# Optimization experiments

Measured on AMD Instinct MI355X. Metric: run time of the kernel, lower is better.

## Reference

```python
import jax, jax.numpy as jnp
import numpy as np

CAMS, HEADS, PTS, LAYERS = 6, 8, 2, 3
D, DH, FFN = 256, 32, 512
VZ, VH, VW = 8, 50, 50
NQ = VZ * VH * VW
IN_C = 768
IMG_H, IMG_W = 256, 704
FH, FW = IMG_H // 32, IMG_W // 32   # 8, 22
L = FH * FW                         # 176 tokens per camera
LVIS = 44                           # visible tokens (mask_ratio=0.75)


def _layer_norm(x, g, b, eps=1e-5):
    m = x.mean(-1, keepdims=True)
    v = x.var(-1, keepdims=True)
    return (x - m) / jnp.sqrt(v + eps) * g + b


def _group_norm(x, g, b, groups=16, eps=1e-5):
    B, C = x.shape[0], x.shape[1]
    xg = x.reshape(B, groups, C // groups, *x.shape[2:])
    m = xg.mean(axis=(2, 3, 4, 5), keepdims=True)
    v = xg.var(axis=(2, 3, 4, 5), keepdims=True)
    xg = (xg - m) / jnp.sqrt(v + eps)
    return xg.reshape(x.shape) * g[None, :, None, None, None] + b[None, :, None, None, None]


def _bilinear(val, loc, Hf, Wf):
    # val: [C, HW, heads, dh]; loc: [C, NQ, heads, P, 2] as (x, y) pixel coords
    x, y = loc[..., 0], loc[..., 1]
    x0 = jnp.floor(x); y0 = jnp.floor(y)
    wx, wy = x - x0, y - y0
    x0i, y0i = x0.astype(jnp.int32), y0.astype(jnp.int32)
    cidx = jnp.arange(val.shape[0])[:, None, None, None]
    hidx = jnp.arange(val.shape[2])[None, None, :, None]

    def g(yi, xi):
        idx = jnp.clip(yi, 0, Hf - 1) * Wf + jnp.clip(xi, 0, Wf - 1)
        return val[cidx, idx, hidx]  # [C,NQ,heads,P,dh]

    out = ((1 - wx) * (1 - wy))[..., None] * g(y0i, x0i)
    out = out + (wx * (1 - wy))[..., None] * g(y0i, x0i + 1)
    out = out + ((1 - wx) * wy)[..., None] * g(y0i + 1, x0i)
    out = out + (wx * wy)[..., None] * g(y0i + 1, x0i + 1)
    return out


def setup_inputs() -> dict:
    key = jax.random.key(0)
    ks = iter(jax.random.split(key, 48))

    def rn(shape, s=0.02):
        return jax.random.normal(next(ks), shape, jnp.float32) * s

    return {
        'camera_x': jax.random.normal(next(ks), (CAMS, LVIS, IN_C), jnp.float32),
        'camera_ids_restore': jax.random.randint(next(ks), (CAMS, L), 0, L),
        'img_h': IMG_H, 'img_w': IMG_W,
        'mask_token': rn((1, 1, IN_C)),
        'vol_emb': rn((NQ, D), 1.0),
        'W_tc': rn((D, IN_C)), 'b_tc': jnp.zeros((D,), jnp.float32),
        'cams_embeds': rn((CAMS, D), 1.0),
        'level_embeds': rn((1, D), 1.0),
        'W_off': rn((LAYERS, D, HEADS * CAMS * PTS * 2)),
        'b_off': rn((LAYERS, HEADS * CAMS * PTS * 2), 2.0),
        'W_att': rn((LAYERS, D, HEADS * CAMS * PTS)),
        'b_att': jnp.zeros((LAYERS, HEADS * CAMS * PTS), jnp.float32),
        'W_val': rn((LAYERS, D, D)), 'b_val': jnp.zeros((LAYERS, D), jnp.float32),
        'W_out': rn((LAYERS, D, D)), 'b_out': jnp.zeros((LAYERS, D), jnp.float32),
        'ln1_g': jnp.ones((LAYERS, D), jnp.float32), 'ln1_b': jnp.zeros((LAYERS, D), jnp.float32),
        'W_ff1': rn((LAYERS, D, FFN)), 'b_ff1': jnp.zeros((LAYERS, FFN), jnp.float32),
        'W_ff2': rn((LAYERS, FFN, D)), 'b_ff2': jnp.zeros((LAYERS, D), jnp.float32),
        'ln2_g': jnp.ones((LAYERS, D), jnp.float32), 'ln2_b': jnp.zeros((LAYERS, D), jnp.float32),
        'deconv_w': rn((D, D, 2, 2, 2)),
        'gn1_g': jnp.ones((D,), jnp.float32), 'gn1_b': jnp.zeros((D,), jnp.float32),
        'conv3_w': rn((192, D, 3, 3, 3)),
        'gn2_g': jnp.ones((192,), jnp.float32), 'gn2_b': jnp.zeros((192,), jnp.float32),
    }


def _forward(camera_x, camera_ids_restore, img_h, img_w, mask_token, vol_emb, W_tc, b_tc,
             cams_embeds, level_embeds, W_off, b_off, W_att, b_att, W_val, b_val, W_out, b_out,
             ln1_g, ln1_b, W_ff1, b_ff1, W_ff2, b_ff2, ln2_g, ln2_b,
             deconv_w, gn1_g, gn1_b, conv3_w, gn2_g, gn2_b):
    N, Lfull = camera_ids_restore.shape
    # 1) MAE unshuffle: append mask tokens, gather back to original order
    mt = jnp.broadcast_to(mask_token, (N, Lfull - camera_x.shape[1], IN_C)).astype(camera_x.dtype)
    full = jnp.concatenate([camera_x, mt], axis=1)                         # [N,L,C]
    full = jnp.take_along_axis(full, camera_ids_restore[:, :, None], axis=1)
    Hf, Wf = img_h // 32, img_w // 32
    cam_x = jnp.transpose(full, (0, 2, 1)).reshape(1, N, IN_C, Hf, Wf)     # [1,6,768,8,22]
    # 2) 1x1 transfer conv + ReLU
    vf = jax.nn.relu(jnp.einsum('bnchw,oc->bnohw', cam_x, W_tc) + b_tc[None, None, :, None, None])
    # 3) flatten spatial + cam/level embeds -> per-camera feature maps [N,HW,D]
    vf = jnp.transpose(vf.reshape(1, N, D, Hf * Wf), (1, 0, 3, 2))          # [N,1,HW,D]
    vf = vf + cams_embeds[:, None, None, :] + level_embeds[None, None, 0:1, :]
    feat = vf[:, 0]                                                         # [N,HW,D]
    # 4) reference points of volume queries (z slow, h, w fast) -> pixel coords
    ww = (jnp.arange(VW, dtype=jnp.float32) + 0.5) / VW
    hh = (jnp.arange(VH, dtype=jnp.float32) + 0.5) / VH
    grid = jnp.stack([jnp.tile(ww, VH), jnp.repeat(hh, VW)], axis=-1)       # [VH*VW,2]
    ref_pix = jnp.tile(grid, (VZ, 1)) * jnp.array([Wf, Hf], jnp.float32) - 0.5  # [NQ,2]
    # 5) deformable cross-attention volume encoder
    q = vol_emb
    for l in range(LAYERS):
        off = (q @ W_off[l] + b_off[l]).reshape(NQ, HEADS, CAMS, PTS, 2)
        att = jax.nn.softmax((q @ W_att[l] + b_att[l]).reshape(NQ, HEADS, CAMS * PTS), axis=-1)
        att = jnp.transpose(att.reshape(NQ, HEADS, CAMS, PTS), (2, 0, 1, 3))      # [C,NQ,H,P]
        val = (feat @ W_val[l] + b_val[l]).reshape(CAMS, Hf * Wf, HEADS, DH)
        loc = jnp.transpose(ref_pix[:, None, None, None, :] + off, (2, 0, 1, 3, 4))  # [C,NQ,H,P,2]
        sampled = _bilinear(val, loc, Hf, Wf)                                     # [C,NQ,H,P,DH]
        agg = jnp.einsum('cnhp,cnhpd->nhd', att, sampled).reshape(NQ, D)
        q = _layer_norm(q + agg @ W_out[l] + b_out[l], ln1_g[l], ln1_b[l])
        q = _layer_norm(q + jax.nn.relu(q @ W_ff1[l] + b_ff1[l]) @ W_ff2[l] + b_ff2[l], ln2_g[l], ln2_b[l])
    # 6) reshape -> [1, D, VW, VH, VZ] (matches .permute(0,4,3,2,1))
    vol = jnp.transpose(q.reshape(1, VZ, VH, VW, D), (0, 4, 3, 2, 1))
    # 7) deblock: deconv3d(k=2,s=2) -> GN16 -> ReLU -> conv3d(k=3,p=1) -> GN16 -> ReLU
    x = jax.lax.conv_transpose(vol, deconv_w, (2, 2, 2), 'VALID',
                               dimension_numbers=('NCDHW', 'OIDHW', 'NCDHW'))
    x = jax.nn.relu(_group_norm(x, gn1_g, gn1_b))
    x = jax.lax.conv_general_dilated(x, conv3_w, (1, 1, 1), [(1, 1)] * 3,
                                     dimension_numbers=('NCDHW', 'OIDHW', 'NCDHW'))
    x = jax.nn.relu(_group_norm(x, gn2_g, gn2_b))
    return x, cam_x


def reference(camera_x, camera_ids_restore, img_h, img_w, mask_token, vol_emb, W_tc, b_tc,
              cams_embeds, level_embeds, W_off, b_off, W_att, b_att, W_val, b_val, W_out, b_out,
              ln1_g, ln1_b, W_ff1, b_ff1, W_ff2, b_ff2, ln2_g, ln2_b,
              deconv_w, gn1_g, gn1_b, conv3_w, gn2_g, gn2_b):
    return _forward(camera_x, camera_ids_restore, img_h, img_w, mask_token, vol_emb, W_tc, b_tc,
                    cams_embeds, level_embeds, W_off, b_off, W_att, b_att, W_val, b_val, W_out, b_out,
                    ln1_g, ln1_b, W_ff1, b_ff1, W_ff2, b_ff2, ln2_g, ln2_b,
                    deconv_w, gn1_g, gn1_b, conv3_w, gn2_g, gn2_b)
```

## Files before the change

### kernel.cpp

```cpp
#include <hip/hip_runtime.h>
#include <stdint.h>

typedef __attribute__((ext_vector_type(8))) short s16x8;
typedef __attribute__((ext_vector_type(4))) float f32x4;

static __device__ __forceinline__ unsigned short f2bf(float f) {
  unsigned u = __float_as_uint(f);
  u += 0x7FFFu + ((u >> 16) & 1u);
  return (unsigned short)(u >> 16);
}
static __device__ __forceinline__ float bf2f(unsigned short h) {
  return __uint_as_float(((unsigned)h) << 16);
}
static __device__ __forceinline__ void sum8(uint4 u, float& a, float& q) {
  unsigned w[4] = {u.x, u.y, u.z, u.w};
#pragma unroll
  for (int i = 0; i < 4; ++i) {
    float v0 = __uint_as_float((w[i] & 0xFFFFu) << 16);
    float v1 = __uint_as_float(w[i] & 0xFFFF0000u);
    a += v0 + v1;
    q += v0 * v0 + v1 * v1;
  }
}

__global__ void k_prep(const float* __restrict__ W_tc, const float* __restrict__ W_val,
                       const float* __restrict__ W_off, const float* __restrict__ W_att,
                       const float* __restrict__ W_out, const float* __restrict__ W_ff1,
                       const float* __restrict__ W_ff2, const float* __restrict__ deconv_w,
                       const float* __restrict__ conv3_w,
                       unsigned short* __restrict__ Wt_tc, unsigned short* __restrict__ Wt_val,
                       unsigned short* __restrict__ Wt_oa, unsigned short* __restrict__ Wt_out,
                       unsigned short* __restrict__ Wt_ff1, unsigned short* __restrict__ Wt_ff2,
                       unsigned short* __restrict__ Wt_dc, unsigned short* __restrict__ wc3) {
  int idx = blockIdx.x * 256 + threadIdx.x;
  if (idx < 196608) { Wt_tc[idx] = f2bf(W_tc[idx]); return; }
  idx -= 196608;
  if (idx < 196608) {
    int l = idx / 65536, r = idx - l * 65536, k = r >> 8, n = r & 255;
    Wt_val[l * 65536 + n * 256 + k] = f2bf(W_val[l * 65536 + r]);
    return;
  }
  idx -= 196608;
  if (idx < 147456) {
    int l = idx / 49152, r = idx - l * 49152, k = r / 192, n = r - k * 192;
    Wt_oa[l * 73728 + n * 256 + k] = f2bf(W_off[l * 49152 + r]);
    return;
  }
  idx -= 147456;
  if (idx < 73728) {
    int l = idx / 24576, r = idx - l * 24576, k = r / 96, n = r - k * 96;
    Wt_oa[l * 73728 + 192 * 256 + n * 256 + k] = f2bf(W_att[l * 24576 + r]);
    return;
  }
  idx -= 73728;
  if (idx < 196608) {
    int l = idx / 65536, r = idx - l * 65536, k = r >> 8, n = r & 255;
    Wt_out[l * 65536 + n * 256 + k] = f2bf(W_out[l * 65536 + r]);
    return;
  }
  idx -= 196608;
  if (idx < 393216) {
    int l = idx / 131072, r = idx - l * 131072, k = r >> 9, n = r & 511;
    Wt_ff1[l * 131072 + n * 256 + k] = f2bf(W_ff1[l * 131072 + r]);
    return;
  }
  idx -= 393216;
  if (idx < 393216) {
    int l = idx / 131072, r = idx - l * 131072, k = r >> 8, n = r & 255;
    Wt_ff2[l * 131072 + n * 512 + k] = f2bf(W_ff2[l * 131072 + r]);
    return;
  }
  idx -= 393216;
  if (idx < 524288) {
    int n = idx >> 8, k = idx & 255;
    Wt_dc[idx] = f2bf(deconv_w[(size_t)(n & 255) * 2048 + k * 8 + (n >> 8)]);
    return;
  }
  idx -= 524288;
  if (idx < 1327104) {
    int tap = idx / 49152;
    int rem = idx - tap * 49152;
    int oc = rem >> 8, ic = rem & 255;
    int chunk = ic >> 5, kg = (ic >> 3) & 3, j = ic & 7;
    int ocblk = oc >> 4, lo = oc & 15;
    size_t frag = (size_t)(tap * 8 + chunk) * 12 + ocblk;
    wc3[(frag * 64 + kg * 16 + lo) * 8 + j] = f2bf(conv3_w[(oc * 256 + ic) * 27 + tap]);
    return;
  }
}

__global__ void k_cvt(const float* __restrict__ in, unsigned short* __restrict__ out, int n) {
  int i = blockIdx.x * 256 + threadIdx.x;
  if (i < n) out[i] = f2bf(in[i]);
}

__global__ void k_restore2(const float* __restrict__ cx, const int* __restrict__ ids,
                           const float* __restrict__ mtok, float* __restrict__ out_camx,
                           unsigned short* __restrict__ camxT) {
  int idx = blockIdx.x * 256 + threadIdx.x;
  if (idx >= 811008) return;
  int ch = idx % 768;
  int row = idx / 768;
  int c = row / 176, p = row - c * 176;
  int id = ids[c * 176 + p];
  float v = (id < 44) ? cx[((size_t)(c * 44 + id)) * 768 + ch] : mtok[ch];
  camxT[idx] = f2bf(v);
  out_camx[((size_t)(c * 768 + ch)) * 176 + p] = v;
}

template <int MODE>
__global__ __launch_bounds__(256) void k_gemm(
    const unsigned short* __restrict__ A, int M, int lda,
    const unsigned short* __restrict__ Bt, int K, int N,
    const float* __restrict__ bias, const float* __restrict__ bias2, int n1, int relu,
    float* __restrict__ Cf, unsigned short* __restrict__ Cb, int ldc,
    const float* __restrict__ cemb, const float* __restrict__ lemb) {
  __shared__ short sA[128 * 40];
  const int t = threadIdx.x;
  const int l = t & 63, w = t >> 6;
  const int lo = l & 15, kg = l >> 4;
  const int row0 = blockIdx.x * 128, n0 = blockIdx.y * 64;
  const s16x8 bz = {0, 0, 0, 0, 0, 0, 0, 0};
  f32x4 acc[2][4] = {};
  s16x8 bc[4], bn[4];
#pragma unroll
  for (int nb = 0; nb < 4; ++nb) {
    int n = n0 + nb * 16 + lo;
    bc[nb] = (n < N) ? *(const s16x8*)&Bt[(size_t)n * K + kg * 8] : bz;
  }
  const int stR = t >> 1, stH = t & 1;
  for (int kc = 0; kc < K; kc += 32) {
    const bool pf = (kc + 32 < K);
    if (pf) {
#pragma unroll
      for (int nb = 0; nb < 4; ++nb) {
        int n = n0 + nb * 16 + lo;
        bn[nb] = (n < N) ? *(const s16x8*)&Bt[(size_t)n * K + kc + 32 + kg * 8] : bz;
      }
    }
    __syncthreads();
    {
      int r = row0 + stR;
      uint4 v0 = {0u, 0u, 0u, 0u}, v1 = {0u, 0u, 0u, 0u};
      if (r < M) {
        const unsigned short* src = A + (size_t)r * lda + kc + stH * 16;
        v0 = *(const uint4*)src;
        v1 = *(const uint4*)(src + 8);
      }
      *(uint4*)&sA[stR * 40 + stH * 16] = v0;
      *(uint4*)&sA[stR * 40 + stH * 16 + 8] = v1;
    }
    __syncthreads();
    s16x8 a0 = *(const s16x8*)&sA[(w * 32 + lo) * 40 + kg * 8];
    s16x8 a1 = *(const s16x8*)&sA[(w * 32 + 16 + lo) * 40 + kg * 8];
#pragma unroll
    for (int nb = 0; nb < 4; ++nb) {
      acc[0][nb] = __builtin_amdgcn_mfma_f32_16x16x32_bf16(a0, bc[nb], acc[0][nb], 0, 0, 0);
      acc[1][nb] = __builtin_amdgcn_mfma_f32_16x16x32_bf16(a1, bc[nb], acc[1][nb], 0, 0, 0);
    }
    if (pf) {
#pragma unroll
      for (int nb = 0; nb < 4; ++nb) bc[nb] = bn[nb];
    }
  }
#pragma unroll
  for (int m = 0; m < 2; ++m)
#pragma unroll
    for (int nb = 0; nb < 4; ++nb)
#pragma unroll
      for (int r = 0; r < 4; ++r) {
        int row = row0 + w * 32 + m * 16 + (kg << 2) + r;
        int col = n0 + nb * 16 + lo;
        if (row < M && col < N) {
          float v = acc[m][nb][r];
          if (bias) v += (col < n1) ? bias[col] : bias2[col - n1];
          if (relu) v = fmaxf(v, 0.f);
          if (MODE == 0) {
            Cf[(size_t)row * ldc + col] = v;
          } else if (MODE == 2) {
            Cb[(size_t)row * ldc + col] = f2bf(v);
          } else {
            v += cemb[(row / 176) * 256 + col] + lemb[col];
            Cb[(size_t)row * ldc + col] = f2bf(v);
          }
        }
      }
}

__global__ __launch_bounds__(256, 2) void k_deconv(const unsigned short* __restrict__ A,
                                                   const unsigned short* __restrict__ Bt,
                                                   unsigned short* __restrict__ Cb, int M) {
  __shared__ short sA[128 * 256];
  const int t = threadIdx.x;
  const int l = t & 63, w = t >> 6;
  const int lo = l & 15, kg = l >> 4;
  const int row0 = blockIdx.x * 128;
#pragma unroll
  for (int i = 0; i < 16; ++i) {
    int g = t + i * 256;
    int row = g >> 5, gcol = g & 31;
    int r = row0 + row;
    uint4 v = {0u, 0u, 0u, 0u};
    if (r < M) v = *(const uint4*)&A[(size_t)r * 256 + gcol * 8];
    *(uint4*)&sA[row * 256 + ((gcol ^ (row & 7)) << 3)] = v;
  }
  __syncthreads();
  const int r0 = w * 32 + lo, r1 = r0 + 16;
  for (int nt = 0; nt < 32; ++nt) {
    f32x4 acc[2][4] = {};
    s16x8 bc[4], bn[4];
    const int ncol0 = nt * 64;
#pragma unroll
    for (int nb = 0; nb < 4; ++nb)
      bc[nb] = *(const s16x8*)&Bt[(size_t)(ncol0 + nb * 16 + lo) * 256 + kg * 8];
#pragma unroll
    for (int kc = 0; kc < 8; ++kc) {
      const bool pf = kc < 7;
      if (pf) {
#pragma unroll
        for (int nb = 0; nb < 4; ++nb)
          bn[nb] = *(const s16x8*)&Bt[(size_t)(ncol0 + nb * 16 + lo) * 256 + (kc + 1) * 32 + kg * 8];
      }
      int g0 = kc * 4 + kg;
      s16x8 a0 = *(const s16x8*)&sA[r0 * 256 + ((g0 ^ (r0 & 7)) << 3)];
      s16x8 a1 = *(const s16x8*)&sA[r1 * 256 + ((g0 ^ (r1 & 7)) << 3)];
#pragma unroll
      for (int nb = 0; nb < 4; ++nb) {
        acc[0][nb] = __builtin_amdgcn_mfma_f32_16x16x32_bf16(a0, bc[nb], acc[0][nb], 0, 0, 0);
        acc[1][nb] = __builtin_amdgcn_mfma_f32_16x16x32_bf16(a1, bc[nb], acc[1][nb], 0, 0, 0);
      }
      if (pf) {
#pragma unroll
        for (int nb = 0; nb < 4; ++nb) bc[nb] = bn[nb];
      }
    }
    const int tap = nt >> 2;
    const int t1 = tap >> 2, t2 = (tap >> 1) & 1, t3 = tap & 1;
#pragma unroll
    for (int m = 0; m < 2; ++m)
#pragma unroll
      for (int nb = 0; nb < 4; ++nb)
#pragma unroll
        for (int r = 0; r < 4; ++r) {
          int row = row0 + w * 32 + m * 16 + (kg << 2) + r;
          if (row < M) {
            int oc = (nt & 3) * 64 + nb * 16 + lo;
            int z = row / 2500, rr = row - z * 2500;
            int hy = rr / 50, wx = rr - hy * 50;
            int od = 2 * wx + 1 - t1, oh = 2 * hy + 1 - t2, ow = 2 * z + 1 - t3;
            Cb[((size_t)((od * 100 + oh) * 16 + ow)) * 256 + oc] = f2bf(acc[m][nb][r]);
          }
        }
  }
}

__global__ __launch_bounds__(256) void k_sample(const float* __restrict__ oa,
                                                const float* __restrict__ val,
                                                unsigned short* __restrict__ aggb) {
  __shared__ float sl[96], sw[96];
  int t = threadIdx.x;
  int h = t >> 5, d = t & 31;
  const float* vbh0 = val + (size_t)h * 32 + d;
  for (int r = 0; r < 8; ++r) {
    int n = blockIdx.x * 8 + r;
    if (t < 96) sl[t] = oa[(size_t)n * 288 + 192 + t];
    __syncthreads();
    if (t < 96) {
      int hh = t / 12;
      float mx = -1e30f;
#pragma unroll
      for (int j = 0; j < 12; ++j) mx = fmaxf(mx, sl[hh * 12 + j]);
      sw[t] = __expf(sl[t] - mx);
    }
    __syncthreads();
    float ssum = 0.f;
#pragma unroll
    for (int j = 0; j < 12; ++j) ssum += sw[h * 12 + j];
    float inv = 1.f / ssum;
    float xr = ((float)(n % 50) + 0.5f) * (22.0f / 50.0f) - 0.5f;
    float yr = ((float)((n / 50) % 50) + 0.5f) * (8.0f / 50.0f) - 0.5f;
    float acc = 0.f;
    const float* offn = oa + (size_t)n * 288 + h * 24;
#pragma unroll
    for (int c = 0; c < 6; ++c)
#pragma unroll
      for (int p2 = 0; p2 < 2; ++p2) {
        float x = xr + offn[(c * 2 + p2) * 2];
        float y = yr + offn[(c * 2 + p2) * 2 + 1];
        float x0 = floorf(x), y0 = floorf(y);
        float wx = x - x0, wy = y - y0;
        int ix0 = min(max((int)x0, 0), 21), ix1 = min(max((int)x0 + 1, 0), 21);
        int iy0 = min(max((int)y0, 0), 7), iy1 = min(max((int)y0 + 1, 0), 7);
        const float* vb = vbh0 + (size_t)c * 176 * 768;
        float v00 = vb[(size_t)(iy0 * 22 + ix0) * 768];
        float v01 = vb[(size_t)(iy0 * 22 + ix1) * 768];
        float v10 = vb[(size_t)(iy1 * 22 + ix0) * 768];
        float v11 = vb[(size_t)(iy1 * 22 + ix1) * 768];
        float bil = (1.f - wx) * (1.f - wy) * v00 + wx * (1.f - wy) * v01 +
                    (1.f - wx) * wy * v10 + wx * wy * v11;
        acc += sw[h * 12 + c * 2 + p2] * inv * bil;
      }
    aggb[(size_t)n * 256 + t] = f2bf(acc);
    __syncthreads();
  }
}

__global__ __launch_bounds__(256) void k_addln(float* __restrict__ q, const float* __restrict__ p,
                                               const float* __restrict__ g, const float* __restrict__ b,
                                               unsigned short* __restrict__ qb) {
  __shared__ float red[8];
  int t = threadIdx.x;
  int w = t >> 6;
  float gg = g[t], bb = b[t];
  for (int r = 0; r < 8; ++r) {
    size_t n = (size_t)blockIdx.x * 8 + r;
    float x = q[n * 256 + t] + p[n * 256 + t];
    float s1 = x, s2 = x * x;
#pragma unroll
    for (int o = 32; o >= 1; o >>= 1) {
      s1 += __shfl_xor(s1, o, 64);
      s2 += __shfl_xor(s2, o, 64);
    }
    if ((t & 63) == 0) { red[w * 2] = s1; red[w * 2 + 1] = s2; }
    __syncthreads();
    s1 = red[0] + red[2] + red[4] + red[6];
    s2 = red[1] + red[3] + red[5] + red[7];
    float mean = s1 * (1.0f / 256.0f);
    float var = s2 * (1.0f / 256.0f) - mean * mean;
    float y = (x - mean) * rsqrtf(var + 1e-5f) * gg + bb;
    q[n * 256 + t] = y;
    qb[n * 256 + t] = f2bf(y);
    __syncthreads();
  }
}

__global__ __launch_bounds__(256) void k_gnstat1(const unsigned short* __restrict__ X, float* __restrict__ part) {
  __shared__ float s1[256], s2[256];
  int b = blockIdx.x, t = threadIdx.x;
  int oc8 = t & 31, v0 = t >> 5;
  float a = 0.f, q = 0.f;
#pragma unroll
  for (int i = 0; i < 8; ++i) {
    int vox = v0 + i * 8;
    uint4 u = *(const uint4*)&X[(size_t)b * 16384 + vox * 256 + oc8 * 8];
    sum8(u, a, q);
  }
  s1[t] = a; s2[t] = q;
  __syncthreads();
  if (t < 128) { s1[t] += s1[t + 128]; s2[t] += s2[t + 128]; }
  __syncthreads();
  if (t < 64) { s1[t] += s1[t + 64]; s2[t] += s2[t + 64]; }
  __syncthreads();
  if (t < 32) { s1[t] += s1[t + 32]; s2[t] += s2[t + 32]; }
  __syncthreads();
  if (t < 16) {
    part[t * 2500 + b] = s1[2 * t] + s1[2 * t + 1];
    part[40000 + t * 2500 + b] = s2[2 * t] + s2[2 * t + 1];
  }
}

__global__ __launch_bounds__(256) void k_gnred1(const float* __restrict__ part, float* __restrict__ gmv) {
  __shared__ float s1[256], s2[256];
  int g = blockIdx.x, t = threadIdx.x;
  float a = 0.f, q = 0.f;
  for (int i = t; i < 2500; i += 256) { a += part[g * 2500 + i]; q += part[40000 + g * 2500 + i]; }
  s1[t] = a; s2[t] = q;
  __syncthreads();
  for (int s = 128; s > 0; s >>= 1) {
    if (t < s) { s1[t] += s1[t + s]; s2[t] += s2[t + s]; }
    __syncthreads();
  }
  if (t == 0) {
    float m = s1[0] / 2560000.0f;
    float v = s2[0] / 2560000.0f - m * m;
    gmv[2 * g] = m; gmv[2 * g + 1] = rsqrtf(v + 1e-5f);
  }
}

__global__ __launch_bounds__(256) void k_gnapply1(unsigned short* __restrict__ X, const float* __restrict__ gmv,
                                                  const float* __restrict__ g, const float* __restrict__ b) {
  for (unsigned i = blockIdx.x * 256 + threadIdx.x; i < 5120000u; i += gridDim.x * 256) {
    unsigned e = i * 8u;
    int oc0 = e & 255, grp = oc0 >> 4;
    float mean = gmv[grp * 2], rstd = gmv[grp * 2 + 1];
    float4 g0 = *(const float4*)&g[oc0], g1 = *(const float4*)&g[oc0 + 4];
    float4 b0 = *(const float4*)&b[oc0], b1 = *(const float4*)&b[oc0 + 4];
    uint4 u = *(const uint4*)&X[e];
    unsigned w[4] = {u.x, u.y, u.z, u.w};
    float gg[8] = {g0.x, g0.y, g0.z, g0.w, g1.x, g1.y, g1.z, g1.w};
    float bb[8] = {b0.x, b0.y, b0.z, b0.w, b1.x, b1.y, b1.z, b1.w};
    unsigned o[4];
#pragma unroll
    for (int j = 0; j < 4; ++j) {
      float v0 = __uint_as_float((w[j] & 0xFFFFu) << 16);
      float v1 = __uint_as_float(w[j] & 0xFFFF0000u);
      v0 = fmaxf((v0 - mean) * rstd * gg[2 * j] + bb[2 * j], 0.f);
      v1 = fmaxf((v1 - mean) * rstd * gg[2 * j + 1] + bb[2 * j + 1], 0.f);
      o[j] = (unsigned)f2bf(v0) | ((unsigned)f2bf(v1) << 16);
    }
    *(uint4*)&X[e] = make_uint4(o[0], o[1], o[2], o[3]);
  }
}

__global__ __launch_bounds__(256, 2) void k_conv3(const unsigned short* __restrict__ X,
                                                  const unsigned short* __restrict__ Wp,
                                                  unsigned short* __restrict__ Y) {
  __shared__ short sX[4 * 543 * 8];
  int bid = blockIdx.x;
  int xcd = bid & 7, idx = bid >> 3;
  int swz = (xcd < 4 ? xcd * 163 : 652 + (xcd - 4) * 162) + idx;
  const int od = swz / 13;
  const int oh0 = (swz - od * 13) * 8;
  const int t = threadIdx.x;
  const int l = t & 63, w = t >> 6;
  const int kg = l >> 4, lo = l & 15;
  f32x4 acc[8][3] = {};
  s16x8 bc[9], bn[9];
  const unsigned short* Wl = Wp + (size_t)l * 8;
  const int w3 = w * 3;
#pragma unroll
  for (int t2 = 0; t2 < 3; ++t2)
#pragma unroll
    for (int nb = 0; nb < 3; ++nb)
      bc[t2 * 3 + nb] = *(const s16x8*)&Wl[(size_t)((t2 * 3 * 8) * 12 + w3 + nb) * 512];

  for (int gi = 0; gi < 72; ++gi) {
    const int chunk = gi / 9;
    const int sub = gi - chunk * 9;
    const int t1 = sub / 3, t3 = sub - t1 * 3;
    if (sub == 0) {
      __syncthreads();
#pragma unroll
      for (int i = 0; i < 9; ++i) {
        int e = t + i * 256;
        if (e < 2160) {
          int pos = e >> 2, ks = e & 3;
          int sd = pos / 180, r2 = pos - sd * 180;
          int sh = r2 / 18, sw_ = r2 - sh * 18;
          int gd = od + sd - 1, gh = oh0 + sh - 1, gw = sw_ - 1;
          uint4 v = {0u, 0u, 0u, 0u};
          if ((unsigned)gd < 100u && (unsigned)gh < 100u && (unsigned)gw < 16u)
            v = *(const uint4*)&X[((size_t)((gd * 100 + gh) * 16 + gw)) * 256 + chunk * 32 + ks * 8];
          *(uint4*)&sX[(ks * 543 + pos) * 8] = v;
        }
      }
      __syncthreads();
    }
    const int gn1 = gi + 1;
    if (gn1 < 72) {
      const int c1 = gn1 / 9, su1 = gn1 - c1 * 9;
      const int t1n = su1 / 3, t3n = su1 - t1n * 3;
#pragma unroll
      for (int t2 = 0; t2 < 3; ++t2)
#pragma unroll
        for (int nb = 0; nb < 3; ++nb)
          bn[t2 * 3 + nb] = *(const s16x8*)&Wl[
              (size_t)(((t1n * 9 + t2 * 3 + t3n) * 8 + c1) * 12 + w3 + nb) * 512];
    }
    const int abase = kg * 543 + t1 * 180 + lo + t3;
#pragma unroll
    for (int sh = 0; sh < 10; ++sh) {
      s16x8 a = *(const s16x8*)&sX[(abase + sh * 18) * 8];
#pragma unroll
      for (int t2 = 0; t2 < 3; ++t2) {
        const int m = sh - t2;
        if (m >= 0 && m < 8) {
          acc[m][0] = __builtin_amdgcn_mfma_f32_16x16x32_bf16(a, bc[t2 * 3 + 0], acc[m][0], 0, 0, 0);
          acc[m][1] = __builtin_amdgcn_mfma_f32_16x16x32_bf16(a, bc[t2 * 3 + 1], acc[m][1], 0, 0, 0);
          acc[m][2] = __builtin_amdgcn_mfma_f32_16x16x32_bf16(a, bc[t2 * 3 + 2], acc[m][2], 0, 0, 0);
        }
      }
    }
#pragma unroll
    for (int i = 0; i < 9; ++i) bc[i] = bn[i];
  }
#pragma unroll
  for (int m = 0; m < 8; ++m) {
    int oh = oh0 + m;
    if (oh < 100) {
#pragma unroll
      for (int nb = 0; nb < 3; ++nb)
#pragma unroll
        for (int r = 0; r < 4; ++r) {
          int oc = w * 48 + nb * 16 + lo;
          int ow = (kg << 2) + r;
          Y[(size_t)oc * 160000 + (size_t)((od * 100 + oh) * 16) + ow] = f2bf(acc[m][nb][r]);
        }
    }
  }
}

__global__ __launch_bounds__(256) void k_gnstat2(const unsigned short* __restrict__ X, float* __restrict__ part) {
  __shared__ float s1[256], s2[256];
  int b = blockIdx.x, t = threadIdx.x;
  int ch = b / 10, pp = b - ch * 10;
  const unsigned short* base = X + (size_t)ch * 160000 + (size_t)pp * 16000;
  float a = 0.f, q = 0.f;
  for (int i = t; i < 2000; i += 256) {
    uint4 u = *(const uint4*)&base[i * 8];
    sum8(u, a, q);
  }
  s1[t] = a; s2[t] = q;
  __syncthreads();
  for (int s = 128; s > 0; s >>= 1) {
    if (t < s) { s1[t] += s1[t + s]; s2[t] += s2[t + s]; }
    __syncthreads();
  }
  if (t == 0) { part[80000 + ch * 10 + pp] = s1[0]; part[81920 + ch * 10 + pp] = s2[0]; }
}

__global__ __launch_bounds__(256) void k_gnred2(const float* __restrict__ part, float* __restrict__ gmv) {
  __shared__ float s1[256], s2[256];
  int g = blockIdx.x, t = threadIdx.x;
  float a = (t < 120) ? part[80000 + g * 120 + t] : 0.f;
  float q = (t < 120) ? part[81920 + g * 120 + t] : 0.f;
  s1[t] = a; s2[t] = q;
  __syncthreads();
  for (int s = 128; s > 0; s >>= 1) {
    if (t < s) { s1[t] += s1[t + s]; s2[t] += s2[t + s]; }
    __syncthreads();
  }
  if (t == 0) {
    float m = s1[0] / 1920000.0f;
    float v = s2[0] / 1920000.0f - m * m;
    gmv[2 * g] = m; gmv[2 * g + 1] = rsqrtf(v + 1e-5f);
  }
}

__global__ __launch_bounds__(256) void k_gnapply2(const unsigned short* __restrict__ X, const float* __restrict__ gmv,
                                                  const float* __restrict__ g, const float* __restrict__ b,
                                                  float* __restrict__ out) {
  for (unsigned i = blockIdx.x * 256 + threadIdx.x; i < 3840000u; i += gridDim.x * 256) {
    unsigned oc = i / 20000u;
    unsigned grp = oc / 12u;
    float mean = gmv[grp * 2], rstd = gmv[grp * 2 + 1];
    float gam = g[oc], bet = b[oc];
    unsigned e = i * 8u;
    uint4 u = *(const uint4*)&X[e];
    unsigned wv[4] = {u.x, u.y, u.z, u.w};
    float o[8];
#pragma unroll
    for (int j = 0; j < 4; ++j) {
      float v0 = __uint_as_float((wv[j] & 0xFFFFu) << 16);
      float v1 = __uint_as_float(wv[j] & 0xFFFF0000u);
      o[2 * j] = fmaxf((v0 - mean) * rstd * gam + bet, 0.f);
      o[2 * j + 1] = fmaxf((v1 - mean) * rstd * gam + bet, 0.f);
    }
    *(float4*)&out[e] = make_float4(o[0], o[1], o[2], o[3]);
    *(float4*)&out[e + 4] = make_float4(o[4], o[5], o[6], o[7]);
  }
}

static inline dim3 gemm_grid(int M, int N) { return dim3((M + 127) / 128, (N + 63) / 64); }

extern "C" void kernel_launch(void* const* d_in, const int* in_sizes, int n_in,
                              void* d_out, int out_size, void* d_ws, size_t ws_size,
                              hipStream_t stream) {
  const float* camera_x = (const float*)d_in[0];
  const int* ids = (const int*)d_in[1];
  const float* mask_tok = (const float*)d_in[4];
  const float* vol_emb = (const float*)d_in[5];
  const float* W_tc = (const float*)d_in[6];
  const float* b_tc = (const float*)d_in[7];
  const float* cams_emb = (const float*)d_in[8];
  const float* lvl_emb = (const float*)d_in[9];
  const float* W_off = (const float*)d_in[10];
  const float* b_off = (const float*)d_in[11];
  const float* W_att = (const float*)d_in[12];
  const float* b_att = (const float*)d_in[13];
  const float* W_val = (const float*)d_in[14];
  const float* b_val = (const float*)d_in[15];
  const float* W_out = (const float*)d_in[16];
  const float* b_out = (const float*)d_in[17];
  const float* ln1_g = (const float*)d_in[18];
  const float* ln1_b = (const float*)d_in[19];
  const float* W_ff1 = (const float*)d_in[20];
  const float* b_ff1 = (const float*)d_in[21];
  const float* W_ff2 = (const float*)d_in[22];
  const float* b_ff2 = (const float*)d_in[23];
  const float* ln2_g = (const float*)d_in[24];
  const float* ln2_b = (const float*)d_in[25];
  const float* deconv_w = (const float*)d_in[26];
  const float* gn1_g = (const float*)d_in[27];
  const float* gn1_b = (const float*)d_in[28];
  const float* conv3_w = (const float*)d_in[29];
  const float* gn2_g = (const float*)d_in[30];
  const float* gn2_b = (const float*)d_in[31];

  char* ws = (char*)d_ws;
  float* q             = (float*)(ws + 0);
  unsigned short* qb   = (unsigned short*)(ws + 20480000);
  float* proj          = (float*)(ws + 30720000);
  float* oa            = (float*)(ws + 51200000);
  unsigned short* aggb = (unsigned short*)(ws + 74240000);
  unsigned short* ffhb = (unsigned short*)(ws + 84480000);
  float* val3          = (float*)(ws + 104960000);
  unsigned short* featb= (unsigned short*)(ws + 108204032);
  unsigned short* x1bf = (unsigned short*)(ws + 30720000);
  unsigned short* c3   = (unsigned short*)(ws + 112640000);
  unsigned short* Wt_val = (unsigned short*)(ws + 174080000);
  unsigned short* Wt_oa  = (unsigned short*)(ws + 174473216);
  unsigned short* Wt_out = (unsigned short*)(ws + 174915584);
  unsigned short* Wt_ff1 = (unsigned short*)(ws + 175308800);
  unsigned short* Wt_ff2 = (unsigned short*)(ws + 176095232);
  unsigned short* Wt_dc  = (unsigned short*)(ws + 176881664);
  unsigned short* wc3    = (unsigned short*)(ws + 177930240);
  float* part = (float*)(ws + 180584448);
  float* gmv1 = (float*)(ws + 180920320);
  float* gmv2 = (float*)(ws + 180920448);
  unsigned short* Wt_tc  = (unsigned short*)(ws + 180920576);
  unsigned short* camxT  = (unsigned short*)(ws + 181707008);

  float* out_x = (float*)d_out;
  float* out_camx = out_x + 30720000;

  k_prep<<<13472, 256, 0, stream>>>(W_tc, W_val, W_off, W_att, W_out, W_ff1, W_ff2,
                                    deconv_w, conv3_w,
                                    Wt_tc, Wt_val, Wt_oa, Wt_out, Wt_ff1, Wt_ff2, Wt_dc, wc3);

  k_restore2<<<3168, 256, 0, stream>>>(camera_x, ids, mask_tok, out_camx, camxT);
  k_gemm<4><<<gemm_grid(1056, 256), 256, 0, stream>>>(camxT, 1056, 768, Wt_tc, 768, 256,
                                                      b_tc, nullptr, 256, 1, nullptr, featb, 256,
                                                      cams_emb, lvl_emb);
  hipMemcpyAsync(q, vol_emb, (size_t)20000 * 256 * 4, hipMemcpyDeviceToDevice, stream);
  k_cvt<<<20000, 256, 0, stream>>>(vol_emb, qb, 5120000);

  k_gemm<0><<<gemm_grid(1056, 768), 256, 0, stream>>>(featb, 1056, 256, Wt_val, 256, 768,
                                                      b_val, nullptr, 768, 0, val3, nullptr, 768,
                                                      nullptr, nullptr);

  for (int lyr = 0; lyr < 3; ++lyr) {
    k_gemm<0><<<gemm_grid(20000, 288), 256, 0, stream>>>(qb, 20000, 256, Wt_oa + lyr * 73728, 256, 288,
                                                         b_off + lyr * 192, b_att + lyr * 96, 192, 0,
                                                         oa, nullptr, 288, nullptr, nullptr);
    k_sample<<<2500, 256, 0, stream>>>(oa, val3 + lyr * 256, aggb);
    k_gemm<0><<<gemm_grid(20000, 256), 256, 0, stream>>>(aggb, 20000, 256, Wt_out + lyr * 65536, 256, 256,
                                                         b_out + lyr * 256, nullptr, 256, 0,
                                                         proj, nullptr, 256, nullptr, nullptr);
    k_addln<<<2500, 256, 0, stream>>>(q, proj, ln1_g + lyr * 256, ln1_b + lyr * 256, qb);
    k_gemm<2><<<gemm_grid(20000, 512), 256, 0, stream>>>(qb, 20000, 256, Wt_ff1 + lyr * 131072, 256, 512,
                                                         b_ff1 + lyr * 512, nullptr, 512, 1,
                                                         nullptr, ffhb, 512, nullptr, nullptr);
    k_gemm<0><<<gemm_grid(20000, 256), 256, 0, stream>>>(ffhb, 20000, 512, Wt_ff2 + lyr * 131072, 512, 256,
                                                         b_ff2 + lyr * 256, nullptr, 256, 0,
                                                         proj, nullptr, 256, nullptr, nullptr);
    k_addln<<<2500, 256, 0, stream>>>(q, proj, ln2_g + lyr * 256, ln2_b + lyr * 256, qb);
  }

  k_deconv<<<157, 256, 0, stream>>>(qb, Wt_dc, x1bf, 20000);

  k_gnstat1<<<2500, 256, 0, stream>>>(x1bf, part);
  k_gnred1<<<16, 256, 0, stream>>>(part, gmv1);
  k_gnapply1<<<2048, 256, 0, stream>>>(x1bf, gmv1, gn1_g, gn1_b);

  k_conv3<<<1300, 256, 0, stream>>>(x1bf, wc3, c3);

  k_gnstat2<<<1920, 256, 0, stream>>>(c3, part);
  k_gnred2<<<16, 256, 0, stream>>>(part, gmv2);
  k_gnapply2<<<2048, 256, 0, stream>>>(c3, gmv2, gn2_g, gn2_b, out_x);
}
```

Baseline: 1.431 ms.

## Fuse output/FFN2 GEMMs with residual add and LayerNorm

Adds a GEMM kernel that computes a full 256-wide output row tile per block, then applies bias, residual add and LayerNorm in registers before writing q and its bf16 copy. This replaces the separate GEMM-to-proj plus add-LN kernels for both projections in every layer, removing the fp32 proj round trip and a launch. The first layer reads vol_emb directly as the residual, which also drops the initial device copy. The risks are lower occupancy from 64 accumulators per thread, B operands streamed from global memory with no shared staging, and only 313 blocks in the grid.

Result: slower. 1.600 ms (+11.8%).

```diff
diff --git a/kernel.cpp b/kernel.cpp
--- a/kernel.cpp
+++ b/kernel.cpp
@@ -187,6 +187,104 @@
       }
 }
 
+template <int KT>
+__global__ __launch_bounds__(256) void k_gemmln(
+    const unsigned short* __restrict__ A, int M,
+    const unsigned short* __restrict__ Bt,
+    const float* __restrict__ bias,
+    const float* __restrict__ qin,
+    const float* __restrict__ g, const float* __restrict__ b,
+    float* __restrict__ qout, unsigned short* __restrict__ qbout) {
+  __shared__ short sA[64 * (KT + 8)];
+  const int t = threadIdx.x;
+  const int l = t & 63, w = t >> 6;
+  const int lo = l & 15, kg = l >> 4;
+  const int row0 = blockIdx.x * 64;
+  f32x4 acc[16] = {};
+#pragma unroll
+  for (int i = 0; i < KT / 32; ++i) {
+    int gr = t + i * 256;
+    int row = gr / (KT / 8), c8 = gr - row * (KT / 8);
+    int r = row0 + row;
+    uint4 v = {0u, 0u, 0u, 0u};
+    if (r < M) v = *(const uint4*)&A[(size_t)r * KT + c8 * 8];
+    *(uint4*)&sA[row * (KT + 8) + c8 * 8] = v;
+  }
+  __syncthreads();
+  const int arow = (w * 16 + lo) * (KT + 8);
+#pragma unroll
+  for (int h = 0; h < 2; ++h) {
+    s16x8 bc[8], bn[8];
+#pragma unroll
+    for (int nb = 0; nb < 8; ++nb)
+      bc[nb] = *(const s16x8*)&Bt[(size_t)(h * 128 + nb * 16 + lo) * KT + kg * 8];
+#pragma unroll
+    for (int kc = 0; kc < KT; kc += 32) {
+      const bool pf = (kc + 32 < KT);
+      if (pf) {
+#pragma unroll
+        for (int nb = 0; nb < 8; ++nb)
+          bn[nb] = *(const s16x8*)&Bt[(size_t)(h * 128 + nb * 16 + lo) * KT + kc + 32 + kg * 8];
+      }
+      s16x8 a = *(const s16x8*)&sA[arow + kc + kg * 8];
+#pragma unroll
+      for (int nb = 0; nb < 8; ++nb)
+        acc[h * 8 + nb] = __builtin_amdgcn_mfma_f32_16x16x32_bf16(a, bc[nb], acc[h * 8 + nb], 0, 0, 0);
+      if (pf) {
+#pragma unroll
+        for (int nb = 0; nb < 8; ++nb) bc[nb] = bn[nb];
+      }
+    }
+  }
+  float s1[4] = {0.f, 0.f, 0.f, 0.f}, s2[4] = {0.f, 0.f, 0.f, 0.f};
+#pragma unroll
+  for (int h = 0; h < 2; ++h)
+#pragma unroll
+    for (int nb = 0; nb < 8; ++nb) {
+      int col = h * 128 + nb * 16 + lo;
+      float bs = bias[col];
+#pragma unroll
+      for (int r = 0; r < 4; ++r) {
+        int row = row0 + w * 16 + (kg << 2) + r;
+        float v = acc[h * 8 + nb][r] + bs;
+        if (row < M) v += qin[(size_t)row * 256 + col];
+        acc[h * 8 + nb][r] = v;
+        s1[r] += v;
+        s2[r] += v * v;
+      }
+    }
+#pragma unroll
+  for (int o = 8; o >= 1; o >>= 1)
+#pragma unroll
+    for (int r = 0; r < 4; ++r) {
+      s1[r] += __shfl_xor(s1[r], o, 64);
+      s2[r] += __shfl_xor(s2[r], o, 64);
+    }
+  float mean[4], rstd[4];
+#pragma unroll
+  for (int r = 0; r < 4; ++r) {
+    mean[r] = s1[r] * (1.0f / 256.0f);
+    float var = s2[r] * (1.0f / 256.0f) - mean[r] * mean[r];
+    rstd[r] = rsqrtf(var + 1e-5f);
+  }
+#pragma unroll
+  for (int h = 0; h < 2; ++h)
+#pragma unroll
+    for (int nb = 0; nb < 8; ++nb) {
+      int col = h * 128 + nb * 16 + lo;
+      float gg = g[col], bb = b[col];
+#pragma unroll
+      for (int r = 0; r < 4; ++r) {
+        int row = row0 + w * 16 + (kg << 2) + r;
+        if (row < M) {
+          float y = (acc[h * 8 + nb][r] - mean[r]) * rstd[r] * gg + bb;
+          qout[(size_t)row * 256 + col] = y;
+          qbout[(size_t)row * 256 + col] = f2bf(y);
+        }
+      }
+    }
+}
+
 __global__ __launch_bounds__(256, 2) void k_deconv(const unsigned short* __restrict__ A,
                                                    const unsigned short* __restrict__ Bt,
                                                    unsigned short* __restrict__ Cb, int M) {
@@ -301,35 +399,6 @@
         acc += sw[h * 12 + c * 2 + p2] * inv * bil;
       }
     aggb[(size_t)n * 256 + t] = f2bf(acc);
-    __syncthreads();
-  }
-}
-
-__global__ __launch_bounds__(256) void k_addln(float* __restrict__ q, const float* __restrict__ p,
-                                               const float* __restrict__ g, const float* __restrict__ b,
-                                               unsigned short* __restrict__ qb) {
-  __shared__ float red[8];
-  int t = threadIdx.x;
-  int w = t >> 6;
-  float gg = g[t], bb = b[t];
-  for (int r = 0; r < 8; ++r) {
-    size_t n = (size_t)blockIdx.x * 8 + r;
-    float x = q[n * 256 + t] + p[n * 256 + t];
-    float s1 = x, s2 = x * x;
-#pragma unroll
-    for (int o = 32; o >= 1; o >>= 1) {
-      s1 += __shfl_xor(s1, o, 64);
-      s2 += __shfl_xor(s2, o, 64);
-    }
-    if ((t & 63) == 0) { red[w * 2] = s1; red[w * 2 + 1] = s2; }
-    __syncthreads();
-    s1 = red[0] + red[2] + red[4] + red[6];
-    s2 = red[1] + red[3] + red[5] + red[7];
-    float mean = s1 * (1.0f / 256.0f);
-    float var = s2 * (1.0f / 256.0f) - mean * mean;
-    float y = (x - mean) * rsqrtf(var + 1e-5f) * gg + bb;
-    q[n * 256 + t] = y;
-    qb[n * 256 + t] = f2bf(y);
     __syncthreads();
   }
 }
@@ -590,7 +659,6 @@
   char* ws = (char*)d_ws;
   float* q             = (float*)(ws + 0);
   unsigned short* qb   = (unsigned short*)(ws + 20480000);
-  float* proj          = (float*)(ws + 30720000);
   float* oa            = (float*)(ws + 51200000);
   unsigned short* aggb = (unsigned short*)(ws + 74240000);
   unsigned short* ffhb = (unsigned short*)(ws + 84480000);
@@ -622,7 +690,6 @@
   k_gemm<4><<<gemm_grid(1056, 256), 256, 0, stream>>>(camxT, 1056, 768, Wt_tc, 768, 256,
                                                       b_tc, nullptr, 256, 1, nullptr, featb, 256,
                                                       cams_emb, lvl_emb);
-  hipMemcpyAsync(q, vol_emb, (size_t)20000 * 256 * 4, hipMemcpyDeviceToDevice, stream);
   k_cvt<<<20000, 256, 0, stream>>>(vol_emb, qb, 5120000);
 
   k_gemm<0><<<gemm_grid(1056, 768), 256, 0, stream>>>(featb, 1056, 256, Wt_val, 256, 768,
@@ -634,17 +701,14 @@
                                                          b_off + lyr * 192, b_att + lyr * 96, 192, 0,
                                                          oa, nullptr, 288, nullptr, nullptr);
     k_sample<<<2500, 256, 0, stream>>>(oa, val3 + lyr * 256, aggb);
-    k_gemm<0><<<gemm_grid(20000, 256), 256, 0, stream>>>(aggb, 20000, 256, Wt_out + lyr * 65536, 256, 256,
-                                                         b_out + lyr * 256, nullptr, 256, 0,
-                                                         proj, nullptr, 256, nullptr, nullptr);
-    k_addln<<<2500, 256, 0, stream>>>(q, proj, ln1_g + lyr * 256, ln1_b + lyr * 256, qb);
+    k_gemmln<256><<<313, 256, 0, stream>>>(aggb, 20000, Wt_out + lyr * 65536, b_out + lyr * 256,
+                                           (lyr == 0) ? vol_emb : q,
+                                           ln1_g + lyr * 256, ln1_b + lyr * 256, q, qb);
     k_gemm<2><<<gemm_grid(20000, 512), 256, 0, stream>>>(qb, 20000, 256, Wt_ff1 + lyr * 131072, 256, 512,
                                                          b_ff1 + lyr * 512, nullptr, 512, 1,
                                                          nullptr, ffhb, 512, nullptr, nullptr);
-    k_gemm<0><<<gemm_grid(20000, 256), 256, 0, stream>>>(ffhb, 20000, 512, Wt_ff2 + lyr * 131072, 512, 256,
-                                                         b_ff2 + lyr * 256, nullptr, 256, 0,
-                                                         proj, nullptr, 256, nullptr, nullptr);
-    k_addln<<<2500, 256, 0, stream>>>(q, proj, ln2_g + lyr * 256, ln2_b + lyr * 256, qb);
+    k_gemmln<512><<<313, 256, 0, stream>>>(ffhb, 20000, Wt_ff2 + lyr * 131072, b_ff2 + lyr * 256,
+                                           q, ln2_g + lyr * 256, ln2_b + lyr * 256, q, qb);
   }
 
   k_deconv<<<157, 256, 0, stream>>>(qb, Wt_dc, x1bf, 20000);
```

## Fuse GroupNorm statistics into deconv and conv3 epilogues via atomics

Applied to the files above, without the earlier changes.

Computes the per-group sum and sum of squares for both GroupNorms inside the deconv and conv3 epilogues. Partials are reduced within each wave and block, then atomically added to a small global accumulator. A tiny finalize kernel replaces the separate stat and reduce kernels. This drops two full re-reads of the large bf16 intermediates and four launches. In exchange it adds atomic contention, extra registers in the GEMM epilogues, and float atomics that make the summation order nondeterministic.

Result: slower. 1.501 ms (+4.9%).

```diff
diff --git a/kernel.cpp b/kernel.cpp
--- a/kernel.cpp
+++ b/kernel.cpp
@@ -11,16 +11,6 @@
 }
 static __device__ __forceinline__ float bf2f(unsigned short h) {
   return __uint_as_float(((unsigned)h) << 16);
-}
-static __device__ __forceinline__ void sum8(uint4 u, float& a, float& q) {
-  unsigned w[4] = {u.x, u.y, u.z, u.w};
-#pragma unroll
-  for (int i = 0; i < 4; ++i) {
-    float v0 = __uint_as_float((w[i] & 0xFFFFu) << 16);
-    float v1 = __uint_as_float(w[i] & 0xFFFF0000u);
-    a += v0 + v1;
-    q += v0 * v0 + v1 * v1;
-  }
 }
 
 __global__ void k_prep(const float* __restrict__ W_tc, const float* __restrict__ W_val,
@@ -92,6 +82,16 @@
 __global__ void k_cvt(const float* __restrict__ in, unsigned short* __restrict__ out, int n) {
   int i = blockIdx.x * 256 + threadIdx.x;
   if (i < n) out[i] = f2bf(in[i]);
+}
+
+__global__ void k_zero(float* __restrict__ p) { p[threadIdx.x] = 0.f; }
+
+__global__ void k_gnfin(const float* __restrict__ acc, float* __restrict__ gmv, float inv_n) {
+  int t = threadIdx.x;
+  float m = acc[2 * t] * inv_n;
+  float v = acc[2 * t + 1] * inv_n - m * m;
+  gmv[2 * t] = m;
+  gmv[2 * t + 1] = rsqrtf(v + 1e-5f);
 }
 
 __global__ void k_restore2(const float* __restrict__ cx, const int* __restrict__ ids,
@@ -189,7 +189,8 @@
 
 __global__ __launch_bounds__(256, 2) void k_deconv(const unsigned short* __restrict__ A,
                                                    const unsigned short* __restrict__ Bt,
-                                                   unsigned short* __restrict__ Cb, int M) {
+                                                   unsigned short* __restrict__ Cb, int M,
+                                                   float* __restrict__ gnacc) {
   __shared__ short sA[128 * 256];
   const int t = threadIdx.x;
   const int l = t & 63, w = t >> 6;
@@ -206,52 +207,75 @@
   }
   __syncthreads();
   const int r0 = w * 32 + lo, r1 = r0 + 16;
-  for (int nt = 0; nt < 32; ++nt) {
-    f32x4 acc[2][4] = {};
-    s16x8 bc[4], bn[4];
-    const int ncol0 = nt * 64;
-#pragma unroll
-    for (int nb = 0; nb < 4; ++nb)
-      bc[nb] = *(const s16x8*)&Bt[(size_t)(ncol0 + nb * 16 + lo) * 256 + kg * 8];
-#pragma unroll
-    for (int kc = 0; kc < 8; ++kc) {
-      const bool pf = kc < 7;
-      if (pf) {
+  float gs1[16], gs2[16];
+#pragma unroll
+  for (int g = 0; g < 16; ++g) { gs1[g] = 0.f; gs2[g] = 0.f; }
+  for (int ntH = 0; ntH < 8; ++ntH) {
+#pragma unroll
+    for (int ntL = 0; ntL < 4; ++ntL) {
+      const int nt = ntH * 4 + ntL;
+      f32x4 acc[2][4] = {};
+      s16x8 bc[4], bn[4];
+      const int ncol0 = nt * 64;
+#pragma unroll
+      for (int nb = 0; nb < 4; ++nb)
+        bc[nb] = *(const s16x8*)&Bt[(size_t)(ncol0 + nb * 16 + lo) * 256 + kg * 8];
+#pragma unroll
+      for (int kc = 0; kc < 8; ++kc) {
+        const bool pf = kc < 7;
+        if (pf) {
+#pragma unroll
+          for (int nb = 0; nb < 4; ++nb)
+            bn[nb] = *(const s16x8*)&Bt[(size_t)(ncol0 + nb * 16 + lo) * 256 + (kc + 1) * 32 + kg * 8];
+        }
+        int g0 = kc * 4 + kg;
+        s16x8 a0 = *(const s16x8*)&sA[r0 * 256 + ((g0 ^ (r0 & 7)) << 3)];
+        s16x8 a1 = *(const s16x8*)&sA[r1 * 256 + ((g0 ^ (r1 & 7)) << 3)];
+#pragma unroll
+        for (int nb = 0; nb < 4; ++nb) {
+          acc[0][nb] = __builtin_amdgcn_mfma_f32_16x16x32_bf16(a0, bc[nb], acc[0][nb], 0, 0, 0);
+          acc[1][nb] = __builtin_amdgcn_mfma_f32_16x16x32_bf16(a1, bc[nb], acc[1][nb], 0, 0, 0);
+        }
+        if (pf) {
+#pragma unroll
+          for (int nb = 0; nb < 4; ++nb) bc[nb] = bn[nb];
+        }
+      }
+      const int t1 = ntH >> 2, t2 = (ntH >> 1) & 1, t3 = ntH & 1;
+#pragma unroll
+      for (int m = 0; m < 2; ++m)
 #pragma unroll
         for (int nb = 0; nb < 4; ++nb)
-          bn[nb] = *(const s16x8*)&Bt[(size_t)(ncol0 + nb * 16 + lo) * 256 + (kc + 1) * 32 + kg * 8];
-      }
-      int g0 = kc * 4 + kg;
-      s16x8 a0 = *(const s16x8*)&sA[r0 * 256 + ((g0 ^ (r0 & 7)) << 3)];
-      s16x8 a1 = *(const s16x8*)&sA[r1 * 256 + ((g0 ^ (r1 & 7)) << 3)];
-#pragma unroll
-      for (int nb = 0; nb < 4; ++nb) {
-        acc[0][nb] = __builtin_amdgcn_mfma_f32_16x16x32_bf16(a0, bc[nb], acc[0][nb], 0, 0, 0);
-        acc[1][nb] = __builtin_amdgcn_mfma_f32_16x16x32_bf16(a1, bc[nb], acc[1][nb], 0, 0, 0);
-      }
-      if (pf) {
-#pragma unroll
-        for (int nb = 0; nb < 4; ++nb) bc[nb] = bn[nb];
-      }
-    }
-    const int tap = nt >> 2;
-    const int t1 = tap >> 2, t2 = (tap >> 1) & 1, t3 = tap & 1;
-#pragma unroll
-    for (int m = 0; m < 2; ++m)
-#pragma unroll
-      for (int nb = 0; nb < 4; ++nb)
-#pragma unroll
-        for (int r = 0; r < 4; ++r) {
-          int row = row0 + w * 32 + m * 16 + (kg << 2) + r;
-          if (row < M) {
-            int oc = (nt & 3) * 64 + nb * 16 + lo;
-            int z = row / 2500, rr = row - z * 2500;
-            int hy = rr / 50, wx = rr - hy * 50;
-            int od = 2 * wx + 1 - t1, oh = 2 * hy + 1 - t2, ow = 2 * z + 1 - t3;
-            Cb[((size_t)((od * 100 + oh) * 16 + ow)) * 256 + oc] = f2bf(acc[m][nb][r]);
+#pragma unroll
+          for (int r = 0; r < 4; ++r) {
+            int row = row0 + w * 32 + m * 16 + (kg << 2) + r;
+            float v = acc[m][nb][r];
+            gs1[ntL * 4 + nb] += v;
+            gs2[ntL * 4 + nb] += v * v;
+            if (row < M) {
+              int oc = ntL * 64 + nb * 16 + lo;
+              int z = row / 2500, rr = row - z * 2500;
+              int hy = rr / 50, wx = rr - hy * 50;
+              int od = 2 * wx + 1 - t1, oh = 2 * hy + 1 - t2, ow = 2 * z + 1 - t3;
+              Cb[((size_t)((od * 100 + oh) * 16 + ow)) * 256 + oc] = f2bf(v);
+            }
           }
-        }
-  }
+    }
+  }
+  __syncthreads();
+  float* red = (float*)sA;
+#pragma unroll
+  for (int g = 0; g < 16; ++g) {
+    float a = gs1[g], qq = gs2[g];
+#pragma unroll
+    for (int o = 32; o >= 1; o >>= 1) {
+      a += __shfl_xor(a, o, 64);
+      qq += __shfl_xor(qq, o, 64);
+    }
+    if (l == 0) { red[w * 32 + g * 2] = a; red[w * 32 + g * 2 + 1] = qq; }
+  }
+  __syncthreads();
+  if (t < 32) atomicAdd(&gnacc[t], red[t] + red[32 + t] + red[64 + t] + red[96 + t]);
 }
 
 __global__ __launch_bounds__(256) void k_sample(const float* __restrict__ oa,
@@ -334,49 +358,6 @@
   }
 }
 
-__global__ __launch_bounds__(256) void k_gnstat1(const unsigned short* __restrict__ X, float* __restrict__ part) {
-  __shared__ float s1[256], s2[256];
-  int b = blockIdx.x, t = threadIdx.x;
-  int oc8 = t & 31, v0 = t >> 5;
-  float a = 0.f, q = 0.f;
-#pragma unroll
-  for (int i = 0; i < 8; ++i) {
-    int vox = v0 + i * 8;
-    uint4 u = *(const uint4*)&X[(size_t)b * 16384 + vox * 256 + oc8 * 8];
-    sum8(u, a, q);
-  }
-  s1[t] = a; s2[t] = q;
-  __syncthreads();
-  if (t < 128) { s1[t] += s1[t + 128]; s2[t] += s2[t + 128]; }
-  __syncthreads();
-  if (t < 64) { s1[t] += s1[t + 64]; s2[t] += s2[t + 64]; }
-  __syncthreads();
-  if (t < 32) { s1[t] += s1[t + 32]; s2[t] += s2[t + 32]; }
-  __syncthreads();
-  if (t < 16) {
-    part[t * 2500 + b] = s1[2 * t] + s1[2 * t + 1];
-    part[40000 + t * 2500 + b] = s2[2 * t] + s2[2 * t + 1];
-  }
-}
-
-__global__ __launch_bounds__(256) void k_gnred1(const float* __restrict__ part, float* __restrict__ gmv) {
-  __shared__ float s1[256], s2[256];
-  int g = blockIdx.x, t = threadIdx.x;
-  float a = 0.f, q = 0.f;
-  for (int i = t; i < 2500; i += 256) { a += part[g * 2500 + i]; q += part[40000 + g * 2500 + i]; }
-  s1[t] = a; s2[t] = q;
-  __syncthreads();
-  for (int s = 128; s > 0; s >>= 1) {
-    if (t < s) { s1[t] += s1[t + s]; s2[t] += s2[t + s]; }
-    __syncthreads();
-  }
-  if (t == 0) {
-    float m = s1[0] / 2560000.0f;
-    float v = s2[0] / 2560000.0f - m * m;
-    gmv[2 * g] = m; gmv[2 * g + 1] = rsqrtf(v + 1e-5f);
-  }
-}
-
 __global__ __launch_bounds__(256) void k_gnapply1(unsigned short* __restrict__ X, const float* __restrict__ gmv,
                                                   const float* __restrict__ g, const float* __restrict__ b) {
   for (unsigned i = blockIdx.x * 256 + threadIdx.x; i < 5120000u; i += gridDim.x * 256) {
@@ -404,7 +385,8 @@
 
 __global__ __launch_bounds__(256, 2) void k_conv3(const unsigned short* __restrict__ X,
                                                   const unsigned short* __restrict__ Wp,
-                                                  unsigned short* __restrict__ Y) {
+                                                  unsigned short* __restrict__ Y,
+                                                  float* __restrict__ gnacc) {
   __shared__ short sX[4 * 543 * 8];
   int bid = blockIdx.x;
   int xcd = bid & 7, idx = bid >> 3;
@@ -474,6 +456,11 @@
 #pragma unroll
     for (int i = 0; i < 9; ++i) bc[i] = bn[i];
   }
+  __syncthreads();
+  float* lb = (float*)sX;
+  if (t < 32) lb[t] = 0.f;
+  __syncthreads();
+  float cs1[3] = {0.f, 0.f, 0.f}, cs2[3] = {0.f, 0.f, 0.f};
 #pragma unroll
   for (int m = 0; m < 8; ++m) {
     int oh = oh0 + m;
@@ -484,47 +471,26 @@
         for (int r = 0; r < 4; ++r) {
           int oc = w * 48 + nb * 16 + lo;
           int ow = (kg << 2) + r;
-          Y[(size_t)oc * 160000 + (size_t)((od * 100 + oh) * 16) + ow] = f2bf(acc[m][nb][r]);
+          float v = acc[m][nb][r];
+          cs1[nb] += v;
+          cs2[nb] += v * v;
+          Y[(size_t)oc * 160000 + (size_t)((od * 100 + oh) * 16) + ow] = f2bf(v);
         }
     }
   }
-}
-
-__global__ __launch_bounds__(256) void k_gnstat2(const unsigned short* __restrict__ X, float* __restrict__ part) {
-  __shared__ float s1[256], s2[256];
-  int b = blockIdx.x, t = threadIdx.x;
-  int ch = b / 10, pp = b - ch * 10;
-  const unsigned short* base = X + (size_t)ch * 160000 + (size_t)pp * 16000;
-  float a = 0.f, q = 0.f;
-  for (int i = t; i < 2000; i += 256) {
-    uint4 u = *(const uint4*)&base[i * 8];
-    sum8(u, a, q);
-  }
-  s1[t] = a; s2[t] = q;
+#pragma unroll
+  for (int nb = 0; nb < 3; ++nb) {
+    float a = cs1[nb], qq = cs2[nb];
+    a += __shfl_xor(a, 16, 64); qq += __shfl_xor(qq, 16, 64);
+    a += __shfl_xor(a, 32, 64); qq += __shfl_xor(qq, 32, 64);
+    if (kg == 0) {
+      int grp = (w * 48 + nb * 16 + lo) / 12;
+      atomicAdd(&lb[grp * 2], a);
+      atomicAdd(&lb[grp * 2 + 1], qq);
+    }
+  }
   __syncthreads();
-  for (int s = 128; s > 0; s >>= 1) {
-    if (t < s) { s1[t] += s1[t + s]; s2[t] += s2[t + s]; }
-    __syncthreads();
-  }
-  if (t == 0) { part[80000 + ch * 10 + pp] = s1[0]; part[81920 + ch * 10 + pp] = s2[0]; }
-}
-
-__global__ __launch_bounds__(256) void k_gnred2(const float* __restrict__ part, float* __restrict__ gmv) {
-  __shared__ float s1[256], s2[256];
-  int g = blockIdx.x, t = threadIdx.x;
-  float a = (t < 120) ? part[80000 + g * 120 + t] : 0.f;
-  float q = (t < 120) ? part[81920 + g * 120 + t] : 0.f;
-  s1[t] = a; s2[t] = q;
-  __syncthreads();
-  for (int s = 128; s > 0; s >>= 1) {
-    if (t < s) { s1[t] += s1[t + s]; s2[t] += s2[t + s]; }
-    __syncthreads();
-  }
-  if (t == 0) {
-    float m = s1[0] / 1920000.0f;
-    float v = s2[0] / 1920000.0f - m * m;
-    gmv[2 * g] = m; gmv[2 * g + 1] = rsqrtf(v + 1e-5f);
-  }
+  if (t < 32) atomicAdd(&gnacc[t], lb[t]);
 }
 
 __global__ __launch_bounds__(256) void k_gnapply2(const unsigned short* __restrict__ X, const float* __restrict__ gmv,
@@ -605,15 +571,16 @@
   unsigned short* Wt_ff2 = (unsigned short*)(ws + 176095232);
   unsigned short* Wt_dc  = (unsigned short*)(ws + 176881664);
   unsigned short* wc3    = (unsigned short*)(ws + 177930240);
-  float* part = (float*)(ws + 180584448);
   float* gmv1 = (float*)(ws + 180920320);
   float* gmv2 = (float*)(ws + 180920448);
   unsigned short* Wt_tc  = (unsigned short*)(ws + 180920576);
   unsigned short* camxT  = (unsigned short*)(ws + 181707008);
+  float* gnacc = (float*)(ws + 183329024);
 
   float* out_x = (float*)d_out;
   float* out_camx = out_x + 30720000;
 
+  k_zero<<<1, 64, 0, stream>>>(gnacc);
   k_prep<<<13472, 256, 0, stream>>>(W_tc, W_val, W_off, W_att, W_out, W_ff1, W_ff2,
                                     deconv_w, conv3_w,
                                     Wt_tc, Wt_val, Wt_oa, Wt_out, Wt_ff1, Wt_ff2, Wt_dc, wc3);
@@ -647,15 +614,11 @@
     k_addln<<<2500, 256, 0, stream>>>(q, proj, ln2_g + lyr * 256, ln2_b + lyr * 256, qb);
   }
 
-  k_deconv<<<157, 256, 0, stream>>>(qb, Wt_dc, x1bf, 20000);
-
-  k_gnstat1<<<2500, 256, 0, stream>>>(x1bf, part);
-  k_gnred1<<<16, 256, 0, stream>>>(part, gmv1);
+  k_deconv<<<157, 256, 0, stream>>>(qb, Wt_dc, x1bf, 20000, gnacc);
+  k_gnfin<<<1, 16, 0, stream>>>(gnacc, gmv1, 1.0f / 2560000.0f);
   k_gnapply1<<<2048, 256, 0, stream>>>(x1bf, gmv1, gn1_g, gn1_b);
 
-  k_conv3<<<1300, 256, 0, stream>>>(x1bf, wc3, c3);
-
-  k_gnstat2<<<1920, 256, 0, stream>>>(c3, part);
-  k_gnred2<<<16, 256, 0, stream>>>(part, gmv2);
+  k_conv3<<<1300, 256, 0, stream>>>(x1bf, wc3, c3, gnacc + 32);
+  k_gnfin<<<1, 16, 0, stream>>>(gnacc + 32, gmv2, 1.0f / 1920000.0f);
   k_gnapply2<<<2048, 256, 0, stream>>>(c3, gmv2, gn2_g, gn2_b, out_x);
 }
```
